# Performance work log

Hardware: AMD Instinct MI355X
Metric: run time of the kernel (lower is better)

The kernel has to match this reference:

```python
import jax, jax.numpy as jnp
import numpy as np

K = 5  # number of nearest neighbors (module default)


def setup_inputs() -> dict:
    key = jax.random.key(0)
    k1, k2 = jax.random.split(key)
    source_pc = jax.random.normal(k1, (2, 8192, 3), dtype=jnp.float32)
    target_pc = jax.random.normal(k2, (2, 8192, 3), dtype=jnp.float32)
    return {"source_pc": source_pc, "target_pc": target_pc}


def _valid_mask(pc_flat):
    # point is valid if any coordinate is nonzero (move_zero_point)
    return jnp.any(pc_flat != 0.0, axis=-1)


def reference(source_pc, target_pc):
    # move_zero_point flattens all batches into one batch-1 cloud; we emulate
    # the filtering with masks (invalid targets -> +inf distance, invalid
    # sources excluded from the mean) to stay jit-compatible.
    src = source_pc.reshape(-1, 3)   # [Ms, 3] query points
    tgt = target_pc.reshape(-1, 3)   # [Nt, 3] reference points
    src_mask = _valid_mask(src)      # [Ms]
    tgt_mask = _valid_mask(tgt)      # [Nt]

    # squared pairwise distances: |s|^2 + |t|^2 - 2 s.t  -> [Ms, Nt]
    s2 = jnp.sum(src * src, axis=-1)[:, None]
    t2 = jnp.sum(tgt * tgt, axis=-1)[None, :]
    d2 = s2 + t2 - 2.0 * jnp.einsum('md,nd->mn', src, tgt)
    d = jnp.sqrt(jnp.maximum(d2, 1e-12))

    BIG = jnp.float32(1e10)
    d = jnp.where(tgt_mask[None, :], d, BIG)  # drop zero target points

    # k smallest distances per source point (knn returns Euclidean dists)
    neg_topk, _ = jax.lax.top_k(-d, K)        # [Ms, K]
    knn_d = -neg_topk

    # mean over valid source points only
    w = src_mask.astype(knn_d.dtype)
    total = jnp.sum(knn_d * w[:, None])
    count = jnp.sum(w) * K
    return total / count
```

## Files before the change

kernel.cpp:

```cpp
#include <hip/hip_runtime.h>
#include <math.h>

#define KNN 5
#define BLOCK 256

#define G 28
#define NC (G * G * G)
#define NCPAD 24576
#define GRANGE 6.0f
#define H (2.0f * GRANGE / (float)G)
#define INVH ((float)G / (2.0f * GRANGE))
#define LPS 16
#define SPC (BLOCK / LPS)
#define QBLOCKS 512

#define TILE_T 2048
#define WAVES_PER_BLOCK (BLOCK / 64)
#define SRCW 8
#define SRC_PER_BLOCK (WAVES_PER_BLOCK * SRCW)
#define NSPLIT 2

__device__ __forceinline__ float vmin(float a, float b) {
    float r;
    asm("v_min_f32 %0, %1, %2" : "=v"(r) : "v"(a), "v"(b));
    return r;
}
__device__ __forceinline__ float vmax(float a, float b) {
    float r;
    asm("v_max_f32 %0, %1, %2" : "=v"(r) : "v"(a), "v"(b));
    return r;
}

#define INS5(K0, K1, K2, K3, K4, V)                                       \
    do {                                                                  \
        float _v = (V);                                                   \
        K4 = __builtin_amdgcn_fmed3f(K3, K4, _v);                         \
        K3 = __builtin_amdgcn_fmed3f(K2, K3, _v);                         \
        K2 = __builtin_amdgcn_fmed3f(K1, K2, _v);                         \
        K1 = __builtin_amdgcn_fmed3f(K0, K1, _v);                         \
        K0 = vmin(K0, _v);                                                \
    } while (0)

#define MERGE55(a0, a1, a2, a3, a4, b0, b1, b2, b3, b4)                   \
    do {                                                                  \
        float r0 = vmin(a0, b0);                                          \
        float r1 = vmin(vmin(a1, b1), vmax(a0, b0));                      \
        float r2 = vmin(vmin(a2, b2), vmin(vmax(a0, b1), vmax(a1, b0)));  \
        float r3 = vmin(vmin(a3, b3),                                     \
                        vmin(vmax(a0, b2), vmin(vmax(a1, b1), vmax(a2, b0)))); \
        float r4 = vmin(vmin(a4, b4),                                     \
                        vmin(vmin(vmax(a0, b3), vmax(a1, b2)),            \
                             vmin(vmax(a2, b1), vmax(a3, b0))));          \
        a0 = r0; a1 = r1; a2 = r2; a3 = r3; a4 = r4;                      \
    } while (0)

__global__ void finalize_kernel(const float* acc, float* out) {
    out[0] = acc[0] / (acc[1] * (float)KNN);
}
__global__ void init_acc_kernel(float* acc) { acc[0] = 0.0f; acc[1] = 0.0f; }


__device__ __forceinline__ int cell_of(float x, float y, float z) {
    int cx = (int)floorf((x + GRANGE) * INVH);
    int cy = (int)floorf((y + GRANGE) * INVH);
    int cz = (int)floorf((z + GRANGE) * INVH);
    cx = min(max(cx, 0), G - 1);
    cy = min(max(cy, 0), G - 1);
    cz = min(max(cz, 0), G - 1);
    return (cz * G + cy) * G + cx;
}

__global__ void bin_count_kernel(const float* __restrict__ src,
                                 const float* __restrict__ tgt,
                                 int ms, int nt,
                                 int* __restrict__ cnt_s,
                                 int* __restrict__ cnt_t) {
    int i = blockIdx.x * blockDim.x + threadIdx.x;
    int n = ms + nt;
    for (; i < n; i += gridDim.x * blockDim.x) {
        bool isT = (i >= ms);
        const float* p = isT ? (tgt + 3 * (size_t)(i - ms)) : (src + 3 * (size_t)i);
        float x = p[0], y = p[1], z = p[2];
        if (isT && x == 0.0f && y == 0.0f && z == 0.0f) continue;
        atomicAdd((isT ? cnt_t : cnt_s) + cell_of(x, y, z), 1);
    }
}

__global__ __launch_bounds__(1024) void scan_kernel(int* ct, int* ot, int* cs, int* os) {
    __shared__ int psum[1024];
    int* c = blockIdx.x ? cs : ct;
    int* o = blockIdx.x ? os : ot;
    const int t = threadIdx.x;
    int4 v[6];
    const int4* c4 = reinterpret_cast<const int4*>(c) + t * 6;
#pragma unroll
    for (int j = 0; j < 6; ++j) v[j] = c4[j];
    int s = 0;
#pragma unroll
    for (int j = 0; j < 6; ++j) s += v[j].x + v[j].y + v[j].z + v[j].w;
    psum[t] = s;
    __syncthreads();
    for (int d = 1; d < 1024; d <<= 1) {
        int x = (t >= d) ? psum[t - d] : 0;
        __syncthreads();
        psum[t] += x;
        __syncthreads();
    }
    int run = t ? psum[t - 1] : 0;
    int4* o4 = reinterpret_cast<int4*>(o) + t * 6;
    int4* cc4 = reinterpret_cast<int4*>(c) + t * 6;
#pragma unroll
    for (int j = 0; j < 6; ++j) {
        int4 w;
        w.x = run; run += v[j].x;
        w.y = run; run += v[j].y;
        w.z = run; run += v[j].z;
        w.w = run; run += v[j].w;
        o4[j] = w;
        cc4[j] = w;
    }
    if (t == 1023) o[NCPAD] = run;
}

__global__ void scatter_kernel(const float* __restrict__ src,
                               const float* __restrict__ tgt,
                               int ms, int nt,
                               int* __restrict__ cur_s, int* __restrict__ cur_t,
                               float4* __restrict__ pts_s,
                               float4* __restrict__ pts_t) {
    int i = blockIdx.x * blockDim.x + threadIdx.x;
    int n = ms + nt;
    for (; i < n; i += gridDim.x * blockDim.x) {
        bool isT = (i >= ms);
        const float* p = isT ? (tgt + 3 * (size_t)(i - ms)) : (src + 3 * (size_t)i);
        float x = p[0], y = p[1], z = p[2];
        if (isT && x == 0.0f && y == 0.0f && z == 0.0f) continue;
        int cell = cell_of(x, y, z);
        int slot = atomicAdd((isT ? cur_t : cur_s) + cell, 1);
        float w = fmaf(x, x, fmaf(y, y, z * z));
        (isT ? pts_t : pts_s)[slot] = make_float4(x, y, z, w);
    }
}

__global__ __launch_bounds__(BLOCK) void knn_query_kernel(
        const float4* __restrict__ pts_s, const float4* __restrict__ pts_t,
        const int* __restrict__ off_t, float* __restrict__ acc,
        int* __restrict__ tail, int* __restrict__ tailcnt, int ms, int nchunk) {
    __shared__ float redS[4], redC[4];

    const int tid = threadIdx.x;
    const int g = tid >> 4;
    const int m = tid & 15;
    float tsum = 0.0f, tcnt = 0.0f;

    for (int c = blockIdx.x; c < nchunk; c += gridDim.x) {
        const int sidx = c * SPC + g;
        const bool live = (sidx < ms);

        float4 sp = pts_s[live ? sidx : 0];
        const float s2 = sp.w;
        const float nx = -2.0f * sp.x, ny = -2.0f * sp.y, nz = -2.0f * sp.z;

        int cx = (int)floorf((sp.x + GRANGE) * INVH);
        int cy = (int)floorf((sp.y + GRANGE) * INVH);
        int cz = (int)floorf((sp.z + GRANGE) * INVH);
        cx = min(max(cx, 0), G - 1);
        cy = min(max(cy, 0), G - 1);
        cz = min(max(cz, 0), G - 1);
        const int xlo = max(cx - 1, 0), xhi = min(cx + 1, G - 1);
        const float y0 = -GRANGE + cy * H, y1 = y0 + H;
        const float z0 = -GRANGE + cz * H, z1 = z0 + H;

        const int DY[9] = {0, -1, 1, 0, 0, -1, -1, 1, 1};
        const int DZ[9] = {0, 0, 0, -1, 1, -1, 1, -1, 1};
        int rst[9], ren[9];
        float rb[9];
#pragma unroll
        for (int r = 0; r < 9; ++r) {
            const int yy = cy + DY[r], zz = cz + DZ[r];
            const bool ok = ((unsigned)yy < G) && ((unsigned)zz < G);
            const int base = (zz * G + yy) * G;
            rst[r] = ok ? off_t[base + xlo] : 0;
            ren[r] = ok ? off_t[base + xhi + 1] : 0;
            float dys = (DY[r] < 0) ? (sp.y - y0) : ((DY[r] > 0) ? (y1 - sp.y) : 0.0f);
            float dzs = (DZ[r] < 0) ? (sp.z - z0) : ((DZ[r] > 0) ? (z1 - sp.z) : 0.0f);
            dys = fmaxf(dys, 0.0f);
            dzs = fmaxf(dzs, 0.0f);
            rb[r] = fmaf(dys, dys, dzs * dzs);
        }

        float a0 = 1e20f, a1 = 1e20f, a2 = 1e20f, a3 = 1e20f, a4 = 1e20f;
        float b0 = 1e20f, b1 = 1e20f, b2 = 1e20f, b3 = 1e20f, b4 = 1e20f;

        auto scan_range = [&](int st, int en) {
            for (int i = st + m; i < en; i += 2 * LPS) {
                float4 t1 = pts_t[i];
                int i2 = i + LPS;
                bool h2 = (i2 < en);
                float4 t2 = pts_t[h2 ? i2 : i];
                float qa = fmaf(nx, t1.x, fmaf(ny, t1.y, fmaf(nz, t1.z, t1.w)));
                float qb = h2 ? fmaf(nx, t2.x, fmaf(ny, t2.y, fmaf(nz, t2.z, t2.w)))
                              : 1e20f;
                INS5(a0, a1, a2, a3, a4, qa);
                INS5(b0, b1, b2, b3, b4, qb);
            }
        };

        scan_range(rst[0], ren[0]);

        float lim;
        {
            float m0 = a0, m1 = a1, m2 = a2, m3 = a3, m4 = a4;
            MERGE55(m0, m1, m2, m3, m4, b0, b1, b2, b3, b4);
#pragma unroll
            for (int o = 8; o >= 1; o >>= 1) {
                float c0 = __shfl_xor(m0, o);
                float c1 = __shfl_xor(m1, o);
                float c2 = __shfl_xor(m2, o);
                float c3 = __shfl_xor(m3, o);
                float c4 = __shfl_xor(m4, o);
                MERGE55(m0, m1, m2, m3, m4, c0, c1, c2, c3, c4);
            }
            lim = m4 + s2;
        }

#pragma unroll
        for (int r = 1; r < 9; ++r) {
            if (lim > rb[r]) scan_range(rst[r], ren[r]);
        }

        MERGE55(a0, a1, a2, a3, a4, b0, b1, b2, b3, b4);
#pragma unroll
        for (int o = 8; o >= 1; o >>= 1) {
            float c0 = __shfl_xor(a0, o);
            float c1 = __shfl_xor(a1, o);
            float c2 = __shfl_xor(a2, o);
            float c3 = __shfl_xor(a3, o);
            float c4 = __shfl_xor(a4, o);
            MERGE55(a0, a1, a2, a3, a4, c0, c1, c2, c3, c4);
        }

        if (live && m == 0) {
            const bool valid = (sp.x != 0.0f) || (sp.y != 0.0f) || (sp.z != 0.0f);
            if (valid) {
                const bool inbox = fabsf(sp.x) <= GRANGE &&
                                   fabsf(sp.y) <= GRANGE && fabsf(sp.z) <= GRANGE;
                if (inbox && (a4 + s2 <= H * H)) {
                    tsum += sqrtf(fmaxf(a0 + s2, 1e-12f)) +
                            sqrtf(fmaxf(a1 + s2, 1e-12f)) +
                            sqrtf(fmaxf(a2 + s2, 1e-12f)) +
                            sqrtf(fmaxf(a3 + s2, 1e-12f)) +
                            sqrtf(fmaxf(a4 + s2, 1e-12f));
                    tcnt += 1.0f;
                } else {
                    int ti = atomicAdd(tailcnt, 1);
                    tail[ti] = sidx;
                }
            }
        }
    }

#pragma unroll
    for (int off = 32; off >= 1; off >>= 1) {
        tsum += __shfl_down(tsum, off);
        tcnt += __shfl_down(tcnt, off);
    }
    const int wv = tid >> 6;
    if ((tid & 63) == 0) { redS[wv] = tsum; redC[wv] = tcnt; }
    __syncthreads();
    if (tid == 0) {
        float s = redS[0] + redS[1] + redS[2] + redS[3];
        float c = redC[0] + redC[1] + redC[2] + redC[3];
        if (s != 0.0f || c != 0.0f) {
            atomicAdd(&acc[0], s);
            atomicAdd(&acc[1], c);
        }
    }
}

__global__ __launch_bounds__(BLOCK) void knnB_kernel(
        const float4* __restrict__ pts_s, const float4* __restrict__ pts_t,
        const int* __restrict__ off_t, const int* __restrict__ tail,
        const int* __restrict__ tailcnt, float* __restrict__ acc,
        int* __restrict__ ticket, float* __restrict__ out) {
    __shared__ float bl[4][8];
    const int nv = off_t[NC];
    const int T = *tailcnt;
    const int tid = threadIdx.x;
    const int lane = tid & 63, wv = tid >> 6;
    float bsum = 0.0f, bcnt = 0.0f;

    for (int w = blockIdx.x; w < T; w += gridDim.x) {
        float4 sp = pts_s[tail[w]];
        const float s2 = sp.w;
        const float nx = -2.0f * sp.x, ny = -2.0f * sp.y, nz = -2.0f * sp.z;
        float q0 = 1e20f, q1 = 1e20f, q2 = 1e20f, q3 = 1e20f, q4 = 1e20f;
        for (int i = tid; i < nv; i += BLOCK) {
            float4 t = pts_t[i];
            float q = fmaf(nx, t.x, fmaf(ny, t.y, fmaf(nz, t.z, t.w)));
            INS5(q0, q1, q2, q3, q4, q);
        }
#pragma unroll
        for (int off = 32; off >= 1; off >>= 1) {
            float b0 = __shfl_xor(q0, off);
            float b1 = __shfl_xor(q1, off);
            float b2 = __shfl_xor(q2, off);
            float b3 = __shfl_xor(q3, off);
            float b4 = __shfl_xor(q4, off);
            MERGE55(q0, q1, q2, q3, q4, b0, b1, b2, b3, b4);
        }
        __syncthreads();
        if (lane == 0) {
            bl[wv][0] = q0; bl[wv][1] = q1; bl[wv][2] = q2;
            bl[wv][3] = q3; bl[wv][4] = q4;
        }
        __syncthreads();
        if (tid == 0) {
            float a0 = bl[0][0], a1 = bl[0][1], a2 = bl[0][2], a3 = bl[0][3],
                  a4 = bl[0][4];
#pragma unroll
            for (int k = 1; k < 4; ++k) {
                MERGE55(a0, a1, a2, a3, a4,
                        bl[k][0], bl[k][1], bl[k][2], bl[k][3], bl[k][4]);
            }
            bsum += sqrtf(fmaxf(a0 + s2, 1e-12f)) + sqrtf(fmaxf(a1 + s2, 1e-12f)) +
                    sqrtf(fmaxf(a2 + s2, 1e-12f)) + sqrtf(fmaxf(a3 + s2, 1e-12f)) +
                    sqrtf(fmaxf(a4 + s2, 1e-12f));
            bcnt += 1.0f;
        }
    }

    if (tid == 0) {
        if (bcnt != 0.0f) {
            atomicAdd(&acc[0], bsum);
            atomicAdd(&acc[1], bcnt);
        }
        __threadfence();
        int t = atomicAdd(ticket, 1);
        if (t == (int)gridDim.x - 1) {
            float ss = atomicAdd(&acc[0], 0.0f);
            float cc = atomicAdd(&acc[1], 0.0f);
            out[0] = ss / (cc * (float)KNN);
        }
    }
}


__global__ __launch_bounds__(BLOCK, 4) void knn_split_kernel(
        const float* __restrict__ src, const float* __restrict__ tgt,
        float* __restrict__ partials, int ms, int nt, int nth, int spad) {
    __shared__ __align__(16) float xs[TILE_T];
    __shared__ __align__(16) float ys[TILE_T];
    __shared__ __align__(16) float zs[TILE_T];
    __shared__ __align__(16) float w2[TILE_T];

    const int tid = threadIdx.x;
    const int wv = tid >> 6;
    const int lane = tid & 63;
    const int sbase = (blockIdx.x * WAVES_PER_BLOCK + wv) * SRCW;
    const int half = blockIdx.y;
    const int hbase = half * nth;
    const int hend = min(nt, hbase + nth);

    float nx[SRCW], ny[SRCW], nz[SRCW];
#pragma unroll
    for (int s = 0; s < SRCW; ++s) {
        int sp = sbase + s;
        float x = 0.0f, y = 0.0f, z = 0.0f;
        if (sp < ms) {
            x = src[3 * sp + 0];
            y = src[3 * sp + 1];
            z = src[3 * sp + 2];
        }
        nx[s] = -2.0f * x; ny[s] = -2.0f * y; nz[s] = -2.0f * z;
    }
    float q0[SRCW], q1[SRCW], q2[SRCW], q3[SRCW], q4[SRCW];
#pragma unroll
    for (int s = 0; s < SRCW; ++s) {
        q0[s] = 1e30f; q1[s] = 1e30f; q2[s] = 1e30f; q3[s] = 1e30f; q4[s] = 1e30f;
    }

    for (int t0 = hbase; t0 < hend; t0 += TILE_T) {
        int cnt = min(TILE_T, hend - t0);
        for (int t = tid; t < TILE_T; t += BLOCK) {
            float x = 1e10f, y = 0.0f, z = 0.0f;
            if (t < cnt) {
                x = tgt[3 * (size_t)(t0 + t) + 0];
                y = tgt[3 * (size_t)(t0 + t) + 1];
                z = tgt[3 * (size_t)(t0 + t) + 2];
                if (x == 0.0f && y == 0.0f && z == 0.0f) { x = 1e10f; y = 0.0f; z = 0.0f; }
            }
            xs[t] = x; ys[t] = y; zs[t] = z;
            w2[t] = fmaf(x, x, fmaf(y, y, z * z));
        }
        __syncthreads();
#pragma unroll 2
        for (int i = 0; i < TILE_T / 256; ++i) {
            int t = (i << 8) + (lane << 2);
            float4 x4 = *reinterpret_cast<const float4*>(&xs[t]);
            float4 y4 = *reinterpret_cast<const float4*>(&ys[t]);
            float4 z4 = *reinterpret_cast<const float4*>(&zs[t]);
            float4 w4 = *reinterpret_cast<const float4*>(&w2[t]);
#pragma unroll
            for (int s = 0; s < SRCW; ++s) {
                float qa = fmaf(nx[s], x4.x, fmaf(ny[s], y4.x, fmaf(nz[s], z4.x, w4.x)));
                float qb = fmaf(nx[s], x4.y, fmaf(ny[s], y4.y, fmaf(nz[s], z4.y, w4.y)));
                float qc = fmaf(nx[s], x4.z, fmaf(ny[s], y4.z, fmaf(nz[s], z4.z, w4.z)));
                float qd = fmaf(nx[s], x4.w, fmaf(ny[s], y4.w, fmaf(nz[s], z4.w, w4.w)));
                INS5(q0[s], q1[s], q2[s], q3[s], q4[s], qa);
                INS5(q0[s], q1[s], q2[s], q3[s], q4[s], qb);
                INS5(q0[s], q1[s], q2[s], q3[s], q4[s], qc);
                INS5(q0[s], q1[s], q2[s], q3[s], q4[s], qd);
            }
        }
        __syncthreads();
    }
#pragma unroll
    for (int off = 32; off >= 1; off >>= 1) {
#pragma unroll
        for (int s = 0; s < SRCW; ++s) {
            float b0 = __shfl_xor(q0[s], off);
            float b1 = __shfl_xor(q1[s], off);
            float b2 = __shfl_xor(q2[s], off);
            float b3 = __shfl_xor(q3[s], off);
            float b4 = __shfl_xor(q4[s], off);
            MERGE55(q0[s], q1[s], q2[s], q3[s], q4[s], b0, b1, b2, b3, b4);
        }
    }
    if (lane == 0) {
        float* base = partials + ((size_t)half * spad + sbase) * 8;
#pragma unroll
        for (int s = 0; s < SRCW; ++s) {
            if (sbase + s < ms) {
                *reinterpret_cast<float4*>(base + 8 * s) =
                    make_float4(q0[s], q1[s], q2[s], q3[s]);
                *reinterpret_cast<float4*>(base + 8 * s + 4) =
                    make_float4(q4[s], 0.0f, 0.0f, 0.0f);
            }
        }
    }
}

__global__ __launch_bounds__(BLOCK) void merge_kernel(
        const float* __restrict__ src, const float* __restrict__ partials,
        float* __restrict__ acc, int ms, int spad) {
    __shared__ float red_s[WAVES_PER_BLOCK];
    __shared__ float red_c[WAVES_PER_BLOCK];
    const int tid = threadIdx.x;
    const int sp = blockIdx.x * BLOCK + tid;
    float ssum = 0.0f, scnt = 0.0f;
    if (sp < ms) {
        const float* r0p = partials + (size_t)sp * 8;
        const float* r1p = partials + ((size_t)spad + sp) * 8;
        float4 lo0 = *reinterpret_cast<const float4*>(r0p);
        float a4 = r0p[4];
        float4 lo1 = *reinterpret_cast<const float4*>(r1p);
        float b4 = r1p[4];
        float a0 = lo0.x, a1 = lo0.y, a2 = lo0.z, a3 = lo0.w;
        MERGE55(a0, a1, a2, a3, a4, lo1.x, lo1.y, lo1.z, lo1.w, b4);
        float x = src[3 * sp + 0];
        float y = src[3 * sp + 1];
        float z = src[3 * sp + 2];
        bool valid = (x != 0.0f) || (y != 0.0f) || (z != 0.0f);
        float s2 = fmaf(x, x, fmaf(y, y, z * z));
        if (valid) {
            ssum = sqrtf(fmaxf(a0 + s2, 1e-12f)) + sqrtf(fmaxf(a1 + s2, 1e-12f)) +
                   sqrtf(fmaxf(a2 + s2, 1e-12f)) + sqrtf(fmaxf(a3 + s2, 1e-12f)) +
                   sqrtf(fmaxf(a4 + s2, 1e-12f));
            scnt = 1.0f;
        }
    }
#pragma unroll
    for (int off = 32; off >= 1; off >>= 1) {
        ssum += __shfl_down(ssum, off);
        scnt += __shfl_down(scnt, off);
    }
    if ((tid & 63) == 0) { red_s[tid >> 6] = ssum; red_c[tid >> 6] = scnt; }
    __syncthreads();
    if (tid == 0) {
        float s = 0.0f, c = 0.0f;
#pragma unroll
        for (int i = 0; i < WAVES_PER_BLOCK; ++i) { s += red_s[i]; c += red_c[i]; }
        atomicAdd(&acc[0], s);
        atomicAdd(&acc[1], c);
    }
}


extern "C" void kernel_launch(void* const* d_in, const int* in_sizes, int n_in,
                              void* d_out, int out_size, void* d_ws, size_t ws_size,
                              hipStream_t stream) {
    const float* src = (const float*)d_in[0];
    const float* tgt = (const float*)d_in[1];
    const int ms = in_sizes[0] / 3;
    const int nt = in_sizes[1] / 3;

    char* p = (char*)d_ws;
    auto take = [&p](size_t bytes) {
        char* r = p;
        p += (bytes + 15) & ~(size_t)15;
        return r;
    };
    float* acc    = (float*)take(16);
    int* ticket   = (int*)(acc + 2);
    int* tailcnt  = (int*)(acc + 3);
    int* cnt_t    = (int*)take(NCPAD * sizeof(int));
    int* cnt_s    = (int*)take(NCPAD * sizeof(int));
    const size_t zero_bytes = (size_t)((char*)(cnt_s + NCPAD) - (char*)d_ws);
    int* off_t    = (int*)take((NCPAD + 1) * sizeof(int));
    int* off_s    = (int*)take((NCPAD + 1) * sizeof(int));
    float4* pts_t = (float4*)take((size_t)nt * sizeof(float4));
    float4* pts_s = (float4*)take((size_t)ms * sizeof(float4));
    int* tail     = (int*)take((size_t)ms * sizeof(int));
    const size_t need_grid = (size_t)(p - (char*)d_ws);

    if (ws_size >= need_grid) {
        const int n = ms + nt;
        hipMemsetAsync(d_ws, 0, zero_bytes, stream);
        bin_count_kernel<<<(n + 255) / 256, 256, 0, stream>>>(src, tgt, ms, nt,
                                                              cnt_s, cnt_t);
        scan_kernel<<<2, 1024, 0, stream>>>(cnt_t, off_t, cnt_s, off_s);
        scatter_kernel<<<(n + 255) / 256, 256, 0, stream>>>(src, tgt, ms, nt,
                                                            cnt_s, cnt_t, pts_s, pts_t);
        const int nchunk = (ms + SPC - 1) / SPC;
        knn_query_kernel<<<QBLOCKS, BLOCK, 0, stream>>>(pts_s, pts_t, off_t, acc,
                                                        tail, tailcnt, ms, nchunk);
        knnB_kernel<<<1024, BLOCK, 0, stream>>>(pts_s, pts_t, off_t, tail,
                                                tailcnt, acc, ticket,
                                                (float*)d_out);
        return;
    }

    float* acc2 = (float*)d_ws;
    init_acc_kernel<<<1, 1, 0, stream>>>(acc2);
    const int ngroups = (ms + SRC_PER_BLOCK - 1) / SRC_PER_BLOCK;
    const int spad = ngroups * SRC_PER_BLOCK;
    int nth = (nt + NSPLIT - 1) / NSPLIT;
    nth = (nth + TILE_T - 1) / TILE_T * TILE_T;
    float* partials = (float*)((char*)d_ws + 16);
    dim3 grid(ngroups, NSPLIT);
    knn_split_kernel<<<grid, BLOCK, 0, stream>>>(src, tgt, partials, ms, nt, nth, spad);
    merge_kernel<<<(ms + BLOCK - 1) / BLOCK, BLOCK, 0, stream>>>(src, partials,
                                                                 acc2, ms, spad);
    finalize_kernel<<<1, 1, 0, stream>>>(acc2, (float*)d_out);
}
```

Measured before the change: 98.51 us.

## Replace brute-force tail kNN with per-wave expanding grid-shell search

The fallback kernel for tail source points (those the first grid query could not resolve) previously had a whole block brute-force scan every target point. It now assigns one wave per tail point and walks outward through grid shells around the point's cell, stopping once the fifth-best distance is within the shell's guaranteed radius or the grid is fully covered. This removes full scans over all targets for the tail and launches fewer blocks. In exchange, each shell adds a wave-wide merge, and the loop branches and does irregular cell lookups.

```diff
diff --git a/kernel.cpp b/kernel.cpp
--- a/kernel.cpp
+++ b/kernel.cpp
@@ -13,6 +13,7 @@
 #define LPS 16
 #define SPC (BLOCK / LPS)
 #define QBLOCKS 512
+#define TBLOCKS 128
 
 #define TILE_T 2048
 #define WAVES_PER_BLOCK (BLOCK / 64)
@@ -278,62 +279,112 @@
     }
 }
 
-__global__ __launch_bounds__(BLOCK) void knnB_kernel(
+__global__ __launch_bounds__(BLOCK) void knnT_kernel(
         const float4* __restrict__ pts_s, const float4* __restrict__ pts_t,
         const int* __restrict__ off_t, const int* __restrict__ tail,
         const int* __restrict__ tailcnt, float* __restrict__ acc,
         int* __restrict__ ticket, float* __restrict__ out) {
-    __shared__ float bl[4][8];
-    const int nv = off_t[NC];
+    __shared__ float redS[4], redC[4];
     const int T = *tailcnt;
     const int tid = threadIdx.x;
     const int lane = tid & 63, wv = tid >> 6;
-    float bsum = 0.0f, bcnt = 0.0f;
-
-    for (int w = blockIdx.x; w < T; w += gridDim.x) {
-        float4 sp = pts_s[tail[w]];
+    const int wid = blockIdx.x * WAVES_PER_BLOCK + wv;
+    const int nwaves = gridDim.x * WAVES_PER_BLOCK;
+
+    float wsum = 0.0f, wcnt = 0.0f;
+
+    for (int w = wid; w < T; w += nwaves) {
+        const int sidx = tail[w];
+        float4 sp = pts_s[sidx];
         const float s2 = sp.w;
         const float nx = -2.0f * sp.x, ny = -2.0f * sp.y, nz = -2.0f * sp.z;
-        float q0 = 1e20f, q1 = 1e20f, q2 = 1e20f, q3 = 1e20f, q4 = 1e20f;
-        for (int i = tid; i < nv; i += BLOCK) {
-            float4 t = pts_t[i];
-            float q = fmaf(nx, t.x, fmaf(ny, t.y, fmaf(nz, t.z, t.w)));
-            INS5(q0, q1, q2, q3, q4, q);
-        }
-#pragma unroll
-        for (int off = 32; off >= 1; off >>= 1) {
-            float b0 = __shfl_xor(q0, off);
-            float b1 = __shfl_xor(q1, off);
-            float b2 = __shfl_xor(q2, off);
-            float b3 = __shfl_xor(q3, off);
-            float b4 = __shfl_xor(q4, off);
-            MERGE55(q0, q1, q2, q3, q4, b0, b1, b2, b3, b4);
-        }
-        __syncthreads();
+
+        int cx = (int)floorf((sp.x + GRANGE) * INVH);
+        int cy = (int)floorf((sp.y + GRANGE) * INVH);
+        int cz = (int)floorf((sp.z + GRANGE) * INVH);
+        cx = min(max(cx, 0), G - 1);
+        cy = min(max(cy, 0), G - 1);
+        cz = min(max(cz, 0), G - 1);
+        const bool inbox = fabsf(sp.x) <= GRANGE && fabsf(sp.y) <= GRANGE &&
+                           fabsf(sp.z) <= GRANGE;
+        const int covermax = max(max(max(cx, G - 1 - cx), max(cy, G - 1 - cy)),
+                                 max(cz, G - 1 - cz));
+
+        float a0 = 1e20f, a1 = 1e20f, a2 = 1e20f, a3 = 1e20f, a4 = 1e20f;
+
+        auto scan_cells = [&](int yy, int zz, int xa, int xb) {
+            if ((unsigned)yy >= G || (unsigned)zz >= G) return;
+            xa = max(xa, 0);
+            xb = min(xb, G - 1);
+            if (xa > xb) return;
+            const int base = (zz * G + yy) * G;
+            const int st = off_t[base + xa];
+            const int en = off_t[base + xb + 1];
+            for (int i = st + lane; i < en; i += 64) {
+                float4 t = pts_t[i];
+                float q = fmaf(nx, t.x, fmaf(ny, t.y, fmaf(nz, t.z, t.w)));
+                INS5(a0, a1, a2, a3, a4, q);
+            }
+        };
+
+        for (int r = 0; r < G; ++r) {
+            if (r == 0) {
+                scan_cells(cy, cz, cx, cx);
+            } else {
+                for (int dz = -r; dz <= r; ++dz) {
+                    const int zz = cz + dz;
+                    const bool zperim = (dz == -r || dz == r);
+                    for (int dy = -r; dy <= r; ++dy) {
+                        const int yy = cy + dy;
+                        if (zperim || dy == -r || dy == r) {
+                            scan_cells(yy, zz, cx - r, cx + r);
+                        } else {
+                            scan_cells(yy, zz, cx - r, cx - r);
+                            scan_cells(yy, zz, cx + r, cx + r);
+                        }
+                    }
+                }
+            }
+            float m0 = a0, m1 = a1, m2 = a2, m3 = a3, m4 = a4;
+#pragma unroll
+            for (int o = 32; o >= 1; o >>= 1) {
+                float c0 = __shfl_xor(m0, o);
+                float c1 = __shfl_xor(m1, o);
+                float c2 = __shfl_xor(m2, o);
+                float c3 = __shfl_xor(m3, o);
+                float c4 = __shfl_xor(m4, o);
+                MERGE55(m0, m1, m2, m3, m4, c0, c1, c2, c3, c4);
+            }
+            const float rh = (float)r * H;
+            if ((inbox && (m4 + s2 <= rh * rh)) || r >= covermax) break;
+        }
+
+#pragma unroll
+        for (int o = 32; o >= 1; o >>= 1) {
+            float c0 = __shfl_xor(a0, o);
+            float c1 = __shfl_xor(a1, o);
+            float c2 = __shfl_xor(a2, o);
+            float c3 = __shfl_xor(a3, o);
+            float c4 = __shfl_xor(a4, o);
+            MERGE55(a0, a1, a2, a3, a4, c0, c1, c2, c3, c4);
+        }
+
         if (lane == 0) {
-            bl[wv][0] = q0; bl[wv][1] = q1; bl[wv][2] = q2;
-            bl[wv][3] = q3; bl[wv][4] = q4;
-        }
-        __syncthreads();
-        if (tid == 0) {
-            float a0 = bl[0][0], a1 = bl[0][1], a2 = bl[0][2], a3 = bl[0][3],
-                  a4 = bl[0][4];
-#pragma unroll
-            for (int k = 1; k < 4; ++k) {
-                MERGE55(a0, a1, a2, a3, a4,
-                        bl[k][0], bl[k][1], bl[k][2], bl[k][3], bl[k][4]);
-            }
-            bsum += sqrtf(fmaxf(a0 + s2, 1e-12f)) + sqrtf(fmaxf(a1 + s2, 1e-12f)) +
+            wsum += sqrtf(fmaxf(a0 + s2, 1e-12f)) + sqrtf(fmaxf(a1 + s2, 1e-12f)) +
                     sqrtf(fmaxf(a2 + s2, 1e-12f)) + sqrtf(fmaxf(a3 + s2, 1e-12f)) +
                     sqrtf(fmaxf(a4 + s2, 1e-12f));
-            bcnt += 1.0f;
-        }
-    }
-
+            wcnt += 1.0f;
+        }
+    }
+
+    if (lane == 0) { redS[wv] = wsum; redC[wv] = wcnt; }
+    __syncthreads();
     if (tid == 0) {
-        if (bcnt != 0.0f) {
-            atomicAdd(&acc[0], bsum);
-            atomicAdd(&acc[1], bcnt);
+        float s = redS[0] + redS[1] + redS[2] + redS[3];
+        float c = redC[0] + redC[1] + redC[2] + redC[3];
+        if (s != 0.0f || c != 0.0f) {
+            atomicAdd(&acc[0], s);
+            atomicAdd(&acc[1], c);
         }
         __threadfence();
         int t = atomicAdd(ticket, 1);
@@ -525,9 +576,9 @@
         const int nchunk = (ms + SPC - 1) / SPC;
         knn_query_kernel<<<QBLOCKS, BLOCK, 0, stream>>>(pts_s, pts_t, off_t, acc,
                                                         tail, tailcnt, ms, nchunk);
-        knnB_kernel<<<1024, BLOCK, 0, stream>>>(pts_s, pts_t, off_t, tail,
-                                                tailcnt, acc, ticket,
-                                                (float*)d_out);
+        knnT_kernel<<<TBLOCKS, BLOCK, 0, stream>>>(pts_s, pts_t, off_t, tail,
+                                                   tailcnt, acc, ticket,
+                                                   (float*)d_out);
         return;
     }
 
```

After: 147.9 us. 1.5x slower.
